# Performance work log

Hardware: AMD Instinct MI355X
Metric: run time of the kernel (lower is better)

## Reference

```python
import jax, jax.numpy as jnp
import numpy as np

N = 100000
E = 1600000
F_IN = 256   # 4 * 64 after concat
H = 128

def _glorot(key, shape):
    fan_in, fan_out = shape
    lim = jnp.sqrt(6.0 / (fan_in + fan_out))
    return jax.random.uniform(key, shape, jnp.float32, -lim, lim)

def setup_inputs() -> dict:
    key = jax.random.key(0)
    ks = jax.random.split(key, 32)
    inp = {
        'x': jax.random.normal(ks[0], (N, 64), jnp.float32),
        'diff': jax.random.normal(ks[1], (N, 64), jnp.float32),
        'rec_prev': jax.random.normal(ks[2], (N, 64), jnp.float32),
        'hidden_prev': jax.random.normal(ks[3], (N, 64), jnp.float32),
        'edge_index': jax.random.randint(ks[4], (2, E), 0, N, jnp.int64),
    }
    dims = [(F_IN, H), (H, H), (H, H), (H, 1)]
    for i, (din, dout) in enumerate(dims):
        inp[f'Wl{i}'] = _glorot(ks[5 + 3 * i], (din, dout))  # neighbor (aggr) weight
        inp[f'Wr{i}'] = _glorot(ks[6 + 3 * i], (din, dout))  # root weight
        inp[f'b{i}'] = jnp.zeros((dout,), jnp.float32)
    return inp

def _sage_conv(h, src, dst, Wl, Wr, b):
    # mean aggregation of source-node features at destination nodes (PyG SAGEConv)
    msg_sum = jax.ops.segment_sum(h[src], dst, num_segments=N)        # [N, F]
    cnt = jax.ops.segment_sum(jnp.ones((src.shape[0],), h.dtype), dst, num_segments=N)
    mean = msg_sum / jnp.maximum(cnt, 1.0)[:, None]
    return mean @ Wl + h @ Wr + b

def reference(x, diff, rec_prev, hidden_prev, edge_index,
              Wl0, Wr0, b0, Wl1, Wr1, b1, Wl2, Wr2, b2, Wl3, Wr3, b3):
    src, dst = edge_index[0], edge_index[1]
    h = jnp.concatenate([x, diff, rec_prev, hidden_prev], axis=1)  # [N, 256]
    params = [(Wl0, Wr0, b0), (Wl1, Wr1, b1), (Wl2, Wr2, b2), (Wl3, Wr3, b3)]
    h = _sage_conv(h, src, dst, *params[0])
    for Wl, Wr, b in params[1:]:
        h = jax.nn.relu(h)
        h = _sage_conv(h, src, dst, Wl, Wr, b)
    out = jax.nn.sigmoid(h)          # [N, 1]
    lwp_util = jnp.mean(out)
    return out, lwp_util
```

## Files before the change

kernel.cpp:

```cpp
#include <hip/hip_runtime.h>
#include <hip/hip_bf16.h>

#define NN 100000
#define EE 1600000
#define HH 128
#define NB 391
#define CAP 5120

typedef short bf16x8 __attribute__((ext_vector_type(8)));
typedef short bf16x4 __attribute__((ext_vector_type(4)));
typedef float f32x4  __attribute__((ext_vector_type(4)));

__device__ inline short f2bf(float v) {
    __hip_bfloat16 b = __float2bfloat16(v);
    return *reinterpret_cast<short*>(&b);
}

__global__ __launch_bounds__(512) void zerob_kernel(int* __restrict__ bcur) {
    if (threadIdx.x < NB) bcur[threadIdx.x] = 0;
}

__global__ __launch_bounds__(1024) void scatter_prepw_kernel(
    const int* __restrict__ srcv, const int* __restrict__ dstv,
    int* __restrict__ bcur, int* __restrict__ pairs,
    const float* __restrict__ Wl0, const float* __restrict__ Wr0,
    const float* __restrict__ Wl1, const float* __restrict__ Wr1,
    const float* __restrict__ Wl2, const float* __restrict__ Wr2,
    __hip_bfloat16* __restrict__ WT0, __hip_bfloat16* __restrict__ WT1,
    __hip_bfloat16* __restrict__ WT2) {
    __shared__ int hist[NB];
    __shared__ int base[NB];
    const int t = threadIdx.x;

    if (blockIdx.x >= NB) {
        int id = (blockIdx.x - NB) * 1024 + t;
        if (id < 65536) {
            int k = id & 255, n = id >> 8;
            float v = (n < 128) ? Wl0[(size_t)k * 128 + n]
                                : Wr0[(size_t)k * 128 + (n - 128)];
            WT0[(size_t)n * 256 + k] = __float2bfloat16(v);
        } else {
            id -= 65536;
            int layer = id >> 15;
            int u = id & 32767;
            int k = u & 127, n = u >> 7;
            const float* Wl = layer ? Wl2 : Wl1;
            const float* Wr = layer ? Wr2 : Wr1;
            __hip_bfloat16* WT = layer ? WT2 : WT1;
            float v = (n < 128) ? Wl[(size_t)k * 128 + n]
                                : Wr[(size_t)k * 128 + (n - 128)];
            WT[(size_t)n * 128 + k] = __float2bfloat16(v);
        }
        return;
    }

    for (int j = t; j < NB; j += 1024) hist[j] = 0;
    __syncthreads();

    const int e0 = blockIdx.x * 4096;
    int s[4], d[4], n = 0;
#pragma unroll
    for (int u = 0; u < 4; ++u) {
        int e = e0 + u * 1024 + t;
        if (e < EE) { s[n] = srcv[e]; d[n] = dstv[e]; ++n; }
    }
#pragma unroll
    for (int u = 0; u < 4; ++u)
        if (u < n) atomicAdd(&hist[d[u] >> 8], 1);
    __syncthreads();

    for (int j = t; j < NB; j += 1024)
        base[j] = hist[j] ? atomicAdd(&bcur[j], hist[j]) : 0;
    __syncthreads();
    for (int j = t; j < NB; j += 1024) hist[j] = base[j];
    __syncthreads();

#pragma unroll
    for (int u = 0; u < 4; ++u)
        if (u < n) {
            const int b   = d[u] >> 8;
            const int pos = atomicAdd(&hist[b], 1);
            if (pos < CAP) pairs[b * CAP + pos] = (s[u] << 8) | (d[u] & 255);
        }
}

__global__ __launch_bounds__(256) void finalize_kernel(
    const int* __restrict__ bcur, const int* __restrict__ pairs,
    int* __restrict__ csr, int* __restrict__ beg, int* __restrict__ eend,
    float* __restrict__ inv) {
    __shared__ int cnt[256];
    __shared__ int scn[256];
    __shared__ int cur[256];
    const int b = blockIdx.x, t = threadIdx.x;
    int m = bcur[b];
    if (m > CAP) m = CAP;

    cnt[t] = 0;
    __syncthreads();
    for (int e = t; e < m; e += 256)
        atomicAdd(&cnt[pairs[b * CAP + e] & 255], 1);
    __syncthreads();

    const int v = cnt[t];
    scn[t] = v;
    __syncthreads();
    for (int st = 1; st < 256; st <<= 1) {
        int tv = (t >= st) ? scn[t - st] : 0;
        __syncthreads();
        scn[t] += tv;
        __syncthreads();
    }
    const int myStart = scn[t] - v;
    cur[t] = myStart;
    __syncthreads();

    for (int e = t; e < m; e += 256) {
        const int pk  = pairs[b * CAP + e];
        const int pos = atomicAdd(&cur[pk & 255], 1);
        csr[b * CAP + pos] = pk >> 8;
    }

    const int node = b * 256 + t;
    if (node < NN) {
        beg[node]  = b * CAP + myStart;
        eend[node] = b * CAP + myStart + v;
        inv[node]  = 1.0f / fmaxf((float)v, 1.0f);
    }
}

#define TSW 152
template <int K, bool FIRST>
__global__ __launch_bounds__(256) void gemm_kernel(
    const __hip_bfloat16* hin,
    const float* __restrict__ x0, const float* __restrict__ x1,
    const float* __restrict__ x2, const float* __restrict__ x3,
    const __hip_bfloat16* __restrict__ wt, const float* __restrict__ bias,
    __hip_bfloat16* zout, __hip_bfloat16* __restrict__ rout) {
    __shared__ short lsh[64 * TSW];
    const int t    = threadIdx.x;
    const int w    = t >> 6;
    const int lane = t & 63;
    const int quad = lane >> 4;
    const int l16  = lane & 15;
    const int n0   = blockIdx.x * 32;

    const __hip_bfloat16* afeat[4];
#pragma unroll
    for (int ft = 0; ft < 4; ++ft)
        afeat[ft] = wt + (size_t)(w * 64 + ft * 16 + l16) * K + quad * 8;

    f32x4 acc[4][2];
#pragma unroll
    for (int ft = 0; ft < 4; ++ft)
#pragma unroll
        for (int nt = 0; nt < 2; ++nt)
            acc[ft][nt] = (f32x4){0.f, 0.f, 0.f, 0.f};

    constexpr int NPASS = K / 128;
#pragma unroll
    for (int pass = 0; pass < NPASS; ++pass) {
        if (FIRST) {
            const float* sA = pass ? x2 : x0;
            const float* sB = pass ? x3 : x1;
#pragma unroll
            for (int u = 0; u < 4; ++u) {
                const int id  = u * 256 + t;
                const int row = id >> 5, c4 = (id & 31) * 4;
                const float* s = (c4 < 64) ? sA : sB;
                const float4 v = *(const float4*)&s[(size_t)(n0 + row) * 64 + (c4 & 63)];
                bf16x4 p;
                p[0] = f2bf(v.x); p[1] = f2bf(v.y);
                p[2] = f2bf(v.z); p[3] = f2bf(v.w);
                *(bf16x4*)&lsh[row * TSW + c4] = p;
            }
        } else {
#pragma unroll
            for (int u = 0; u < 2; ++u) {
                const int id  = u * 256 + t;
                const int row = id >> 4, c8 = (id & 15) * 8;
                const bf16x8 v = *(const bf16x8*)&hin[(size_t)(n0 + row) * K + c8];
                *(bf16x8*)&lsh[row * TSW + c8] = v;
            }
        }
        __syncthreads();

#pragma unroll
        for (int kcl = 0; kcl < 4; ++kcl) {
            const int kc = pass * 4 + kcl;
            bf16x8 af[4];
#pragma unroll
            for (int ft = 0; ft < 4; ++ft)
                af[ft] = *(const bf16x8*)(afeat[ft] + kc * 32);
            bf16x8 bf[2];
#pragma unroll
            for (int nt = 0; nt < 2; ++nt)
                bf[nt] = *(const bf16x8*)&lsh[(nt * 16 + l16) * TSW + kcl * 32 + quad * 8];
#pragma unroll
            for (int ft = 0; ft < 4; ++ft)
#pragma unroll
                for (int nt = 0; nt < 2; ++nt)
                    acc[ft][nt] = __builtin_amdgcn_mfma_f32_16x16x32_bf16(
                        af[ft], bf[nt], acc[ft][nt], 0, 0, 0);
        }
        __syncthreads();
    }

    {
        short* reg  = lsh + ((w < 2) ? 0 : 32 * TSW);
        const int fcol = (w & 1) * 64;
#pragma unroll
        for (int ft = 0; ft < 4; ++ft) {
            const int fb = ft * 16 + quad * 4;
            float4 bv = make_float4(0.f, 0.f, 0.f, 0.f);
            if (w >= 2) bv = *(const float4*)&bias[fcol + fb];
#pragma unroll
            for (int nt = 0; nt < 2; ++nt) {
                const f32x4 a = acc[ft][nt];
                bf16x4 p;
                p[0] = f2bf(a[0] + bv.x); p[1] = f2bf(a[1] + bv.y);
                p[2] = f2bf(a[2] + bv.z); p[3] = f2bf(a[3] + bv.w);
                *(bf16x4*)&reg[(nt * 16 + l16) * TSW + fcol + fb] = p;
            }
        }
    }
    __syncthreads();

#pragma unroll
    for (int u = 0; u < 2; ++u) {
        const int id  = u * 256 + t;
        const int row = id >> 4, ch = (id & 15) * 8;
        const int nd  = n0 + row;
        *(bf16x8*)&zout[(size_t)nd * HH + ch] = *(const bf16x8*)&lsh[row * TSW + ch];
        *(bf16x8*)&rout[(size_t)nd * HH + ch] =
            *(const bf16x8*)&lsh[(32 + row) * TSW + ch];
    }
}

template <bool LAST>
__global__ __launch_bounds__(256) void aggregate_kernel(
    const __hip_bfloat16* __restrict__ z, __hip_bfloat16* __restrict__ rio,
    const int* __restrict__ beg, const int* __restrict__ eend,
    const int* __restrict__ csr, const float* __restrict__ inv,
    const float* __restrict__ Wl3, const float* __restrict__ Wr3,
    const float* __restrict__ b3, float* __restrict__ z3,
    float* __restrict__ r3) {
    const int i    = (blockIdx.x * 256 + threadIdx.x) >> 6;
    const int lane = threadIdx.x & 63;
    const int g    = lane >> 4;
    const int l16  = lane & 15;
    if (i >= NN) return;
    const int b0 = beg[i], e0 = eend[i];

    float acc[8];
#pragma unroll
    for (int j = 0; j < 8; ++j) acc[j] = 0.f;

    int e = b0 + g;
    for (; e + 12 < e0; e += 16) {
        const int s0 = csr[e];
        const int s1 = csr[e + 4];
        const int s2 = csr[e + 8];
        const int s3 = csr[e + 12];
        const bf16x8 z0 = *(const bf16x8*)&z[(size_t)s0 * HH + l16 * 8];
        const bf16x8 z1 = *(const bf16x8*)&z[(size_t)s1 * HH + l16 * 8];
        const bf16x8 z2 = *(const bf16x8*)&z[(size_t)s2 * HH + l16 * 8];
        const bf16x8 z3v = *(const bf16x8*)&z[(size_t)s3 * HH + l16 * 8];
        const __hip_bfloat162* p0 = (const __hip_bfloat162*)&z0;
        const __hip_bfloat162* p1 = (const __hip_bfloat162*)&z1;
        const __hip_bfloat162* p2 = (const __hip_bfloat162*)&z2;
        const __hip_bfloat162* p3 = (const __hip_bfloat162*)&z3v;
#pragma unroll
        for (int j = 0; j < 4; ++j) {
            acc[2 * j]     += __bfloat162float(p0[j].x) + __bfloat162float(p1[j].x)
                            + __bfloat162float(p2[j].x) + __bfloat162float(p3[j].x);
            acc[2 * j + 1] += __bfloat162float(p0[j].y) + __bfloat162float(p1[j].y)
                            + __bfloat162float(p2[j].y) + __bfloat162float(p3[j].y);
        }
    }
    for (; e < e0; e += 4) {
        const int s0 = csr[e];
        const bf16x8 z0 = *(const bf16x8*)&z[(size_t)s0 * HH + l16 * 8];
        const __hip_bfloat162* p0 = (const __hip_bfloat162*)&z0;
#pragma unroll
        for (int j = 0; j < 4; ++j) {
            acc[2 * j]     += __bfloat162float(p0[j].x);
            acc[2 * j + 1] += __bfloat162float(p0[j].y);
        }
    }

#pragma unroll
    for (int j = 0; j < 8; ++j) {
        acc[j] += __shfl_xor(acc[j], 16, 64);
        acc[j] += __shfl_xor(acc[j], 32, 64);
    }

    const float iv = inv[i];
    const int   f  = l16 * 8 + g * 2;
    const __hip_bfloat162 rv = *(const __hip_bfloat162*)&rio[(size_t)i * HH + f];
    const float ox = fmaxf(acc[g * 2]     * iv + __bfloat162float(rv.x), 0.f);
    const float oy = fmaxf(acc[g * 2 + 1] * iv + __bfloat162float(rv.y), 0.f);

    if (!LAST) {
        __hip_bfloat162 o;
        o.x = __float2bfloat16(ox);
        o.y = __float2bfloat16(oy);
        *(__hip_bfloat162*)&rio[(size_t)i * HH + f] = o;
    } else {
        const float2 wl = *(const float2*)&Wl3[f];
        const float2 wr = *(const float2*)&Wr3[f];
        float al = ox * wl.x + oy * wl.y;
        float ar = ox * wr.x + oy * wr.y;
#pragma unroll
        for (int m = 32; m; m >>= 1) {
            al += __shfl_xor(al, m, 64);
            ar += __shfl_xor(ar, m, 64);
        }
        if (lane == 0) {
            z3[i] = al;
            r3[i] = ar + b3[0];
        }
    }
}

__global__ __launch_bounds__(256) void final_kernel(
    const float* __restrict__ z3, const float* __restrict__ r3,
    const int* __restrict__ beg, const int* __restrict__ eend,
    const int* __restrict__ csr, const float* __restrict__ inv,
    float* __restrict__ out, float* __restrict__ partial) {
    __shared__ float red[4];
    const int i    = (blockIdx.x * 256 + threadIdx.x) >> 6;
    const int lane = threadIdx.x & 63;
    const int w    = threadIdx.x >> 6;
    float v = 0.f;
    if (i < NN) {
        const int b0 = beg[i], e0 = eend[i];
        float a = 0.f;
        for (int e = b0 + lane; e < e0; e += 64) a += z3[csr[e]];
#pragma unroll
        for (int m = 32; m; m >>= 1) a += __shfl_xor(a, m, 64);
        const float pre = a * inv[i] + r3[i];
        const float s = 1.f / (1.f + __expf(-pre));
        if (lane == 0) { out[i] = s; v = s; }
    }
    if (lane == 0) red[w] = v;
    __syncthreads();
    if (threadIdx.x == 0)
        partial[blockIdx.x] = red[0] + red[1] + red[2] + red[3];
}

__global__ __launch_bounds__(256) void mean_kernel(const float* __restrict__ partial,
                                                   int nb, float* __restrict__ out) {
    __shared__ float lds[256];
    float s = 0.f;
    for (int i = threadIdx.x; i < nb; i += 256) s += partial[i];
    lds[threadIdx.x] = s;
    __syncthreads();
    for (int st = 128; st; st >>= 1) {
        if (threadIdx.x < st) lds[threadIdx.x] += lds[threadIdx.x + st];
        __syncthreads();
    }
    if (threadIdx.x == 0) out[NN] = lds[0] / (float)NN;
}

extern "C" void kernel_launch(void* const* d_in, const int* in_sizes, int n_in,
                              void* d_out, int out_size, void* d_ws, size_t ws_size,
                              hipStream_t stream) {
    const float* x    = (const float*)d_in[0];
    const float* diff = (const float*)d_in[1];
    const float* rec  = (const float*)d_in[2];
    const float* hid  = (const float*)d_in[3];
    const int* edge   = (const int*)d_in[4];
    const int* esrc = edge;
    const int* edst = edge + EE;
    const float* Wl0 = (const float*)d_in[5];
    const float* Wr0 = (const float*)d_in[6];
    const float* b0  = (const float*)d_in[7];
    const float* Wl1 = (const float*)d_in[8];
    const float* Wr1 = (const float*)d_in[9];
    const float* b1  = (const float*)d_in[10];
    const float* Wl2 = (const float*)d_in[11];
    const float* Wr2 = (const float*)d_in[12];
    const float* b2  = (const float*)d_in[13];
    const float* Wl3 = (const float*)d_in[14];
    const float* Wr3 = (const float*)d_in[15];
    const float* b3  = (const float*)d_in[16];
    float* out = (float*)d_out;

    char* w = (char*)d_ws;
    auto alloc = [&](size_t bytes) -> void* {
        void* p = (void*)w;
        w += (bytes + 255) & ~(size_t)255;
        return p;
    };
    __hip_bfloat16* bufA = (__hip_bfloat16*)alloc((size_t)NN * HH * 2);
    __hip_bfloat16* bufB = (__hip_bfloat16*)alloc((size_t)NN * HH * 2);
    __hip_bfloat16* WT0  = (__hip_bfloat16*)alloc((size_t)256 * 256 * 2);
    __hip_bfloat16* WT1  = (__hip_bfloat16*)alloc((size_t)256 * 128 * 2);
    __hip_bfloat16* WT2  = (__hip_bfloat16*)alloc((size_t)256 * 128 * 2);
    int*   pairs   = (int*)alloc((size_t)NB * CAP * 4);
    int*   csr     = (int*)alloc((size_t)NB * CAP * 4);
    int*   bcur    = (int*)alloc((size_t)512 * 4);
    int*   beg     = (int*)alloc((size_t)NN * 4);
    int*   eend    = (int*)alloc((size_t)NN * 4);
    float* inv     = (float*)alloc((size_t)NN * 4);
    float* z3      = (float*)alloc((size_t)NN * 4);
    float* r3      = (float*)alloc((size_t)NN * 4);
    float* partial = (float*)alloc((size_t)25000 * 4);

    const int GB  = NN / 32;
    const int WB  = (NN + 3) / 4;

    zerob_kernel<<<1, 512, 0, stream>>>(bcur);
    scatter_prepw_kernel<<<NB + 128, 1024, 0, stream>>>(
        esrc, edst, bcur, pairs, Wl0, Wr0, Wl1, Wr1, Wl2, Wr2, WT0, WT1, WT2);
    finalize_kernel<<<NB, 256, 0, stream>>>(bcur, pairs, csr, beg, eend, inv);

    gemm_kernel<256, true><<<GB, 256, 0, stream>>>(nullptr, x, diff, rec, hid,
                                                   WT0, b0, bufA, bufB);
    aggregate_kernel<false><<<WB, 256, 0, stream>>>(bufA, bufB, beg, eend, csr, inv,
                                                    nullptr, nullptr, nullptr,
                                                    nullptr, nullptr);

    gemm_kernel<128, false><<<GB, 256, 0, stream>>>(bufB, nullptr, nullptr, nullptr, nullptr,
                                                    WT1, b1, bufB, bufA);
    aggregate_kernel<false><<<WB, 256, 0, stream>>>(bufB, bufA, beg, eend, csr, inv,
                                                    nullptr, nullptr, nullptr,
                                                    nullptr, nullptr);

    gemm_kernel<128, false><<<GB, 256, 0, stream>>>(bufA, nullptr, nullptr, nullptr, nullptr,
                                                    WT2, b2, bufA, bufB);
    aggregate_kernel<true><<<WB, 256, 0, stream>>>(bufA, bufB, beg, eend, csr, inv,
                                                   Wl3, Wr3, b3, z3, r3);

    final_kernel<<<WB, 256, 0, stream>>>(z3, r3, beg, eend, csr, inv, out, partial);
    mean_kernel<<<1, 256, 0, stream>>>(partial, WB, out);
}
```

Baseline: 553.9 us.

## Restructure node GEMM to load activations directly into registers, 64 nodes per block

The GEMM kernel no longer stages input activations through shared memory with block-wide barriers. Each wave now loads its B operands straight from global memory and computes all 128 output features for 32 nodes, splitting Z and R halves across waves, with 64 nodes per block. A third buffer lets inputs and outputs never alias, so restrict qualifiers can be applied, and the output is staged per-wave through a small LDS tile with bounds checks. The cost is more weight-fragment loads and accumulator registers per wave, plus redundant activation loads across the Z and R waves.

After: 583.4 us. 5.3% more time.

```diff
diff --git a/kernel.cpp b/kernel.cpp
--- a/kernel.cpp
+++ b/kernel.cpp
@@ -128,111 +128,100 @@
     }
 }
 
-#define TSW 152
+#define TW2 136
 template <int K, bool FIRST>
 __global__ __launch_bounds__(256) void gemm_kernel(
-    const __hip_bfloat16* hin,
+    const __hip_bfloat16* __restrict__ hin,
     const float* __restrict__ x0, const float* __restrict__ x1,
     const float* __restrict__ x2, const float* __restrict__ x3,
     const __hip_bfloat16* __restrict__ wt, const float* __restrict__ bias,
-    __hip_bfloat16* zout, __hip_bfloat16* __restrict__ rout) {
-    __shared__ short lsh[64 * TSW];
+    __hip_bfloat16* __restrict__ zout, __hip_bfloat16* __restrict__ rout) {
+    __shared__ short lsh[4 * 16 * TW2];
     const int t    = threadIdx.x;
     const int w    = t >> 6;
     const int lane = t & 63;
     const int quad = lane >> 4;
     const int l16  = lane & 15;
-    const int n0   = blockIdx.x * 32;
-
-    const __hip_bfloat16* afeat[4];
-#pragma unroll
-    for (int ft = 0; ft < 4; ++ft)
-        afeat[ft] = wt + (size_t)(w * 64 + ft * 16 + l16) * K + quad * 8;
-
-    f32x4 acc[4][2];
-#pragma unroll
-    for (int ft = 0; ft < 4; ++ft)
+    const bool isr = (w >= 2);
+    const int n0   = blockIdx.x * 64;
+    const int nb   = n0 + (w & 1) * 32;
+
+    const __hip_bfloat16* abase = wt + (size_t)((isr ? 128 : 0) + l16) * K + quad * 8;
+
+    int node[2];
+#pragma unroll
+    for (int nt = 0; nt < 2; ++nt) {
+        int n = nb + nt * 16 + l16;
+        node[nt] = (n > NN - 1) ? (NN - 1) : n;
+    }
+
+    f32x4 acc[8][2];
+#pragma unroll
+    for (int ft = 0; ft < 8; ++ft)
 #pragma unroll
         for (int nt = 0; nt < 2; ++nt)
             acc[ft][nt] = (f32x4){0.f, 0.f, 0.f, 0.f};
 
-    constexpr int NPASS = K / 128;
-#pragma unroll
-    for (int pass = 0; pass < NPASS; ++pass) {
+#pragma unroll
+    for (int kc = 0; kc < K / 32; ++kc) {
+        bf16x8 af[8];
+#pragma unroll
+        for (int ft = 0; ft < 8; ++ft)
+            af[ft] = *(const bf16x8*)(abase + (size_t)(ft * 16) * K + kc * 32);
+
+        bf16x8 bf[2];
         if (FIRST) {
-            const float* sA = pass ? x2 : x0;
-            const float* sB = pass ? x3 : x1;
-#pragma unroll
-            for (int u = 0; u < 4; ++u) {
-                const int id  = u * 256 + t;
-                const int row = id >> 5, c4 = (id & 31) * 4;
-                const float* s = (c4 < 64) ? sA : sB;
-                const float4 v = *(const float4*)&s[(size_t)(n0 + row) * 64 + (c4 & 63)];
-                bf16x4 p;
-                p[0] = f2bf(v.x); p[1] = f2bf(v.y);
-                p[2] = f2bf(v.z); p[3] = f2bf(v.w);
-                *(bf16x4*)&lsh[row * TSW + c4] = p;
+            const float* s = (kc < 2) ? x0 : (kc < 4) ? x1 : (kc < 6) ? x2 : x3;
+            const int scol = (kc & 1) * 32 + quad * 8;
+#pragma unroll
+            for (int nt = 0; nt < 2; ++nt) {
+                const float4 v0 = *(const float4*)&s[(size_t)node[nt] * 64 + scol];
+                const float4 v1 = *(const float4*)&s[(size_t)node[nt] * 64 + scol + 4];
+                bf16x8 bb;
+                bb[0] = f2bf(v0.x); bb[1] = f2bf(v0.y);
+                bb[2] = f2bf(v0.z); bb[3] = f2bf(v0.w);
+                bb[4] = f2bf(v1.x); bb[5] = f2bf(v1.y);
+                bb[6] = f2bf(v1.z); bb[7] = f2bf(v1.w);
+                bf[nt] = bb;
             }
         } else {
 #pragma unroll
-            for (int u = 0; u < 2; ++u) {
-                const int id  = u * 256 + t;
-                const int row = id >> 4, c8 = (id & 15) * 8;
-                const bf16x8 v = *(const bf16x8*)&hin[(size_t)(n0 + row) * K + c8];
-                *(bf16x8*)&lsh[row * TSW + c8] = v;
-            }
-        }
-        __syncthreads();
-
-#pragma unroll
-        for (int kcl = 0; kcl < 4; ++kcl) {
-            const int kc = pass * 4 + kcl;
-            bf16x8 af[4];
-#pragma unroll
-            for (int ft = 0; ft < 4; ++ft)
-                af[ft] = *(const bf16x8*)(afeat[ft] + kc * 32);
-            bf16x8 bf[2];
-#pragma unroll
             for (int nt = 0; nt < 2; ++nt)
-                bf[nt] = *(const bf16x8*)&lsh[(nt * 16 + l16) * TSW + kcl * 32 + quad * 8];
-#pragma unroll
-            for (int ft = 0; ft < 4; ++ft)
-#pragma unroll
-                for (int nt = 0; nt < 2; ++nt)
-                    acc[ft][nt] = __builtin_amdgcn_mfma_f32_16x16x32_bf16(
-                        af[ft], bf[nt], acc[ft][nt], 0, 0, 0);
-        }
-        __syncthreads();
-    }
-
-    {
-        short* reg  = lsh + ((w < 2) ? 0 : 32 * TSW);
-        const int fcol = (w & 1) * 64;
-#pragma unroll
-        for (int ft = 0; ft < 4; ++ft) {
+                bf[nt] = *(const bf16x8*)(hin + (size_t)node[nt] * K + kc * 32 + quad * 8);
+        }
+
+#pragma unroll
+        for (int ft = 0; ft < 8; ++ft)
+#pragma unroll
+            for (int nt = 0; nt < 2; ++nt)
+                acc[ft][nt] = __builtin_amdgcn_mfma_f32_16x16x32_bf16(
+                    af[ft], bf[nt], acc[ft][nt], 0, 0, 0);
+    }
+
+    short* reg = lsh + w * 16 * TW2;
+    __hip_bfloat16* outp = isr ? rout : zout;
+#pragma unroll
+    for (int p = 0; p < 2; ++p) {
+#pragma unroll
+        for (int ft = 0; ft < 8; ++ft) {
             const int fb = ft * 16 + quad * 4;
             float4 bv = make_float4(0.f, 0.f, 0.f, 0.f);
-            if (w >= 2) bv = *(const float4*)&bias[fcol + fb];
-#pragma unroll
-            for (int nt = 0; nt < 2; ++nt) {
-                const f32x4 a = acc[ft][nt];
-                bf16x4 p;
-                p[0] = f2bf(a[0] + bv.x); p[1] = f2bf(a[1] + bv.y);
-                p[2] = f2bf(a[2] + bv.z); p[3] = f2bf(a[3] + bv.w);
-                *(bf16x4*)&reg[(nt * 16 + l16) * TSW + fcol + fb] = p;
-            }
-        }
-    }
-    __syncthreads();
-
-#pragma unroll
-    for (int u = 0; u < 2; ++u) {
-        const int id  = u * 256 + t;
-        const int row = id >> 4, ch = (id & 15) * 8;
-        const int nd  = n0 + row;
-        *(bf16x8*)&zout[(size_t)nd * HH + ch] = *(const bf16x8*)&lsh[row * TSW + ch];
-        *(bf16x8*)&rout[(size_t)nd * HH + ch] =
-            *(const bf16x8*)&lsh[(32 + row) * TSW + ch];
+            if (isr) bv = *(const float4*)&bias[fb];
+            const f32x4 a = acc[ft][p];
+            bf16x4 q;
+            q[0] = f2bf(a[0] + bv.x); q[1] = f2bf(a[1] + bv.y);
+            q[2] = f2bf(a[2] + bv.z); q[3] = f2bf(a[3] + bv.w);
+            *(bf16x4*)&reg[l16 * TW2 + fb] = q;
+        }
+#pragma unroll
+        for (int u = 0; u < 4; ++u) {
+            const int row = u * 4 + quad;
+            const int ch  = l16 * 8;
+            const int g   = nb + p * 16 + row;
+            const bf16x8 v = *(const bf16x8*)&reg[row * TW2 + ch];
+            if (g < NN)
+                *(bf16x8*)&outp[(size_t)g * HH + ch] = v;
+        }
     }
 }
 
@@ -394,6 +383,7 @@
     };
     __hip_bfloat16* bufA = (__hip_bfloat16*)alloc((size_t)NN * HH * 2);
     __hip_bfloat16* bufB = (__hip_bfloat16*)alloc((size_t)NN * HH * 2);
+    __hip_bfloat16* bufZ = (__hip_bfloat16*)alloc((size_t)NN * HH * 2);
     __hip_bfloat16* WT0  = (__hip_bfloat16*)alloc((size_t)256 * 256 * 2);
     __hip_bfloat16* WT1  = (__hip_bfloat16*)alloc((size_t)256 * 128 * 2);
     __hip_bfloat16* WT2  = (__hip_bfloat16*)alloc((size_t)256 * 128 * 2);
@@ -407,7 +397,7 @@
     float* r3      = (float*)alloc((size_t)NN * 4);
     float* partial = (float*)alloc((size_t)25000 * 4);
 
-    const int GB  = NN / 32;
+    const int GB  = (NN + 63) / 64;
     const int WB  = (NN + 3) / 4;
 
     zerob_kernel<<<1, 512, 0, stream>>>(bcur);
@@ -416,20 +406,20 @@
     finalize_kernel<<<NB, 256, 0, stream>>>(bcur, pairs, csr, beg, eend, inv);
 
     gemm_kernel<256, true><<<GB, 256, 0, stream>>>(nullptr, x, diff, rec, hid,
-                                                   WT0, b0, bufA, bufB);
-    aggregate_kernel<false><<<WB, 256, 0, stream>>>(bufA, bufB, beg, eend, csr, inv,
+                                                   WT0, b0, bufZ, bufA);
+    aggregate_kernel<false><<<WB, 256, 0, stream>>>(bufZ, bufA, beg, eend, csr, inv,
                                                     nullptr, nullptr, nullptr,
                                                     nullptr, nullptr);
 
-    gemm_kernel<128, false><<<GB, 256, 0, stream>>>(bufB, nullptr, nullptr, nullptr, nullptr,
-                                                    WT1, b1, bufB, bufA);
-    aggregate_kernel<false><<<WB, 256, 0, stream>>>(bufB, bufA, beg, eend, csr, inv,
+    gemm_kernel<128, false><<<GB, 256, 0, stream>>>(bufA, nullptr, nullptr, nullptr, nullptr,
+                                                    WT1, b1, bufZ, bufB);
+    aggregate_kernel<false><<<WB, 256, 0, stream>>>(bufZ, bufB, beg, eend, csr, inv,
                                                     nullptr, nullptr, nullptr,
                                                     nullptr, nullptr);
 
-    gemm_kernel<128, false><<<GB, 256, 0, stream>>>(bufA, nullptr, nullptr, nullptr, nullptr,
-                                                    WT2, b2, bufA, bufB);
-    aggregate_kernel<true><<<WB, 256, 0, stream>>>(bufA, bufB, beg, eend, csr, inv,
+    gemm_kernel<128, false><<<GB, 256, 0, stream>>>(bufB, nullptr, nullptr, nullptr, nullptr,
+                                                    WT2, b2, bufZ, bufA);
+    aggregate_kernel<true><<<WB, 256, 0, stream>>>(bufZ, bufA, beg, eend, csr, inv,
                                                    Wl3, Wr3, b3, z3, r3);
 
     final_kernel<<<WB, 256, 0, stream>>>(z3, r3, beg, eend, csr, inv, out, partial);
```
